# Kernel tuning notes

Measured on AMD Instinct MI355X. Metric: run time of the kernel, lower is better.

Reference implementation:

```python
import jax, jax.numpy as jnp
import numpy as np

B_, L_, H_, N_ = 8, 1024, 1024, 64

def setup_inputs() -> dict:
    key = jax.random.key(0)
    k1, k2, k3, k4 = jax.random.split(key, 4)
    return {
        "samples": jax.random.normal(k1, (B_, L_, 3 * H_), dtype=jnp.float32),
        "label_one_hot": jax.random.uniform(k2, (B_, L_, N_), dtype=jnp.float32),
        "predict": jax.random.normal(k3, (B_, L_, N_), dtype=jnp.float32),
        "W": jax.random.normal(k4, (H_, 3 * H_), dtype=jnp.float32) * (1.0 / np.sqrt(3 * H_)),
        "b_proj": jnp.zeros((H_,), dtype=jnp.float32),
    }

def reference(samples, label_one_hot, predict, W, b_proj):
    # projection: Linear(3H -> H)
    s = jnp.einsum("blk,hk->blh", samples, W) + b_proj          # [b,L,H]
    # dense similarity graph with diagonal masked out, row-softmax
    graph = jnp.einsum("blh,bmh->blm", s, s)                     # [b,L,L]
    L = graph.shape[1]
    eye = jnp.eye(L, dtype=graph.dtype)
    A = jax.nn.softmax(graph - 1e5 * eye, axis=-1)               # [b,L,L]
    # centered masked labels
    sup = label_one_hot
    row_has = (jnp.sum(sup, axis=-1) > 0.5).astype(sup.dtype)    # [b,L]
    total = jnp.sum(row_has, axis=-1)[:, None]                   # [b,1]
    avg = (jnp.sum(sup, axis=-2) / total)[:, None, :]            # [b,1,N]
    B0 = (sup - avg) * row_has[..., None]                        # [b,L,N]
    # diagonal inverse-degree scaling (elementwise, no dense diag matmul)
    d = 1.0 / (jnp.sum(A, axis=-1) + 1e-10)                      # [b,L]
    P = d[:, :, None] * jnp.swapaxes(A, -1, -2)                  # [b,L,L]
    Db = d[:, :, None] * B0                                      # [b,L,N]
    # 6-step power-iteration scan with residual injection at t==3
    ut = jnp.zeros_like(B0)
    for t in range(1, 7):
        ut = jnp.einsum("blm,bmn->bln", P, ut) + Db
        if t == 3:
            ut = ut + predict  # dropout is identity in eval mode
    return ut

if __name__ == "__main__":
    out = reference(**setup_inputs())
    print(out.shape, out.dtype)
```

## Files before the change

kernel.cpp:

```cpp
#include <hip/hip_runtime.h>


typedef _Float16 f16_t;
typedef f16_t f16x4 __attribute__((ext_vector_type(4)));
typedef f16_t f16x8 __attribute__((ext_vector_type(8)));
typedef float floatx4 __attribute__((ext_vector_type(4)));

__device__ __forceinline__ void async_copy16(const void* g, void* l) {
  __builtin_amdgcn_global_load_lds(
      (const __attribute__((address_space(1))) void*)g,
      (__attribute__((address_space(3))) void*)l, 16, 0, 0);
}

__device__ __forceinline__ f16_t hi_of(float x) { return (f16_t)x; }
__device__ __forceinline__ f16_t lo_of(float x, f16_t h) {
  return (f16_t)(x - (float)h);
}

__global__ __launch_bounds__(256) void prep_kernel(
    const float* __restrict__ W, f16_t* __restrict__ Whi, f16_t* __restrict__ Wlo,
    const float* __restrict__ samples, f16_t* __restrict__ SampH)
{
  const int bx = blockIdx.x, tid = threadIdx.x;
  if (bx < 3072) {
    const int i = bx * 256 + tid;
    float4 v = ((const float4*)W)[i];
    v.x *= 32.f; v.y *= 32.f; v.z *= 32.f; v.w *= 32.f;
    f16x4 h, l;
    f16_t h0 = hi_of(v.x); h[0] = h0; l[0] = lo_of(v.x, h0);
    f16_t h1 = hi_of(v.y); h[1] = h1; l[1] = lo_of(v.y, h1);
    f16_t h2 = hi_of(v.z); h[2] = h2; l[2] = lo_of(v.z, h2);
    f16_t h3 = hi_of(v.w); h[3] = h3; l[3] = lo_of(v.w, h3);
    *(f16x4*)(Whi + (size_t)i * 4) = h;
    *(f16x4*)(Wlo + (size_t)i * 4) = l;
  } else {
    const int i = (bx - 3072) * 256 + tid;
    const float4 v = ((const float4*)samples)[i];
    f16x4 h;
    h[0] = (f16_t)v.x; h[1] = (f16_t)v.y; h[2] = (f16_t)v.z; h[3] = (f16_t)v.w;
    *(f16x4*)(SampH + (size_t)i * 4) = h;
  }
}

struct Frags {
  f16x8 a[8];
  f16x8 bh0, bh1, bl0, bl1;
};

#define DSR(dst_, addr_, OFFSTR_) \
  asm volatile("ds_read_b128 %0, %1 offset:" OFFSTR_ : "=v"(dst_) : "v"(addr_))

__device__ __forceinline__ void read_frags_asm(unsigned sa, unsigned sb,
                                               Frags& f) {
  DSR(f.bh0, sb, "0");
  DSR(f.bh1, sb, "1024");
  DSR(f.bl0, sb, "8192");
  DSR(f.bl1, sb, "9216");
  DSR(f.a[0], sa, "0");
  DSR(f.a[1], sa, "1024");
  DSR(f.a[2], sa, "2048");
  DSR(f.a[3], sa, "3072");
  DSR(f.a[4], sa, "4096");
  DSR(f.a[5], sa, "5120");
  DSR(f.a[6], sa, "6144");
  DSR(f.a[7], sa, "7168");
}

__global__ __launch_bounds__(512, 2) void gemm1_pipe(
    const f16_t* __restrict__ Ag,
    const f16_t* __restrict__ BhG, const f16_t* __restrict__ BlG,
    const float* __restrict__ bias,
    f16_t* __restrict__ Chi, f16_t* __restrict__ Clo,
    int N, int K, float cscale)
{
  __shared__ __align__(16) char smem[131072];

  const int tid = threadIdx.x;
  const int lane = tid & 63;
  const int wave = tid >> 6;
  const int wm = wave >> 2;
  const int wn = wave & 3;
  const int bid0 = blockIdx.y * 8 + blockIdx.x;
  const int xk = bid0 & 7, xj = bid0 >> 3;
  const int m0 = ((xk >> 1) * 8 + (xj >> 2)) * 256;
  const int n0 = ((xk & 1) * 4 + (xj & 3)) * 128;
  const int fr = lane & 15;
  const int lch = lane >> 4;

  const int gA0 = tid;
  const int gA1 = tid + 512;
  const int rA0 = gA0 >> 2, lcA0 = (gA0 & 3) ^ ((rA0 >> 1) & 3);
  const int rA1 = gA1 >> 2, lcA1 = (gA1 & 3) ^ ((rA1 >> 1) & 3);
  const int rB = tid >> 2, lcB = (tid & 3) ^ ((rB >> 1) & 3);
  const f16_t* aSrc0 = Ag + (size_t)(m0 + rA0) * K + lcA0 * 8;
  const f16_t* aSrc1 = Ag + (size_t)(m0 + rA1) * K + lcA1 * 8;
  const f16_t* bhSrc = BhG + (size_t)(n0 + rB) * K + lcB * 8;
  const f16_t* blSrc = BlG + (size_t)(n0 + rB) * K + lcB * 8;
  char* ldsA0 = smem + gA0 * 16;
  char* ldsA1 = smem + gA1 * 16;
  char* ldsBh = smem + 16384 + (size_t)tid * 16;
  char* ldsBl = smem + 24576 + (size_t)tid * 16;

  const int swz = (lch ^ ((fr >> 1) & 3)) * 16;
  const int aoff = (wm * 128 + fr) * 64 + swz;
  const int boff = (wn * 32 + fr) * 64 + swz;
  const unsigned ldsBase =
      (unsigned)(size_t)(__attribute__((address_space(3))) char*)smem;
  const unsigned aA0 = ldsBase + (unsigned)aoff;
  const unsigned aA1 = aA0 + 32768u;
  const unsigned aA2 = aA0 + 65536u;
  const unsigned aA3 = aA0 + 98304u;
  const unsigned bA0 = ldsBase + 16384u + (unsigned)boff;
  const unsigned bA1 = bA0 + 32768u;
  const unsigned bA2 = bA0 + 65536u;
  const unsigned bA3 = bA0 + 98304u;

  floatx4 acc[8][2] = {};
  const int NS = K >> 5;

#define STAGE(SS_, SLOT_)                                     \
  do {                                                        \
    int ss = (SS_); if (ss >= NS) ss -= NS;                   \
    const int k0 = ss * 32;                                   \
    async_copy16(aSrc0 + k0, ldsA0 + (SLOT_) * 32768);        \
    async_copy16(aSrc1 + k0, ldsA1 + (SLOT_) * 32768);        \
    async_copy16(bhSrc + k0, ldsBh + (SLOT_) * 32768);        \
    async_copy16(blSrc + k0, ldsBl + (SLOT_) * 32768);        \
  } while (0)

#define MFMA8(F_, P_)                                                                                               \
  do {                                                                                                              \
    acc[2*(P_)][0]   = __builtin_amdgcn_mfma_f32_16x16x32_f16((F_).a[2*(P_)],   (F_).bh0, acc[2*(P_)][0],   0,0,0); \
    acc[2*(P_)][1]   = __builtin_amdgcn_mfma_f32_16x16x32_f16((F_).a[2*(P_)],   (F_).bh1, acc[2*(P_)][1],   0,0,0); \
    acc[2*(P_)+1][0] = __builtin_amdgcn_mfma_f32_16x16x32_f16((F_).a[2*(P_)+1], (F_).bh0, acc[2*(P_)+1][0], 0,0,0); \
    acc[2*(P_)+1][1] = __builtin_amdgcn_mfma_f32_16x16x32_f16((F_).a[2*(P_)+1], (F_).bh1, acc[2*(P_)+1][1], 0,0,0); \
    acc[2*(P_)][0]   = __builtin_amdgcn_mfma_f32_16x16x32_f16((F_).a[2*(P_)],   (F_).bl0, acc[2*(P_)][0],   0,0,0); \
    acc[2*(P_)][1]   = __builtin_amdgcn_mfma_f32_16x16x32_f16((F_).a[2*(P_)],   (F_).bl1, acc[2*(P_)][1],   0,0,0); \
    acc[2*(P_)+1][0] = __builtin_amdgcn_mfma_f32_16x16x32_f16((F_).a[2*(P_)+1], (F_).bl0, acc[2*(P_)+1][0], 0,0,0); \
    acc[2*(P_)+1][1] = __builtin_amdgcn_mfma_f32_16x16x32_f16((F_).a[2*(P_)+1], (F_).bl1, acc[2*(P_)+1][1], 0,0,0); \
  } while (0)

#define SB0 __builtin_amdgcn_sched_barrier(0)

#define HALF(SPRE_, SLOTPRE_, ARD_, BRD_, FRD_, FMM_)            \
  do {                                                           \
    STAGE(SPRE_, SLOTPRE_);                                      \
    asm volatile("s_waitcnt vmcnt(8)" ::: "memory");             \
    __builtin_amdgcn_s_barrier();                                \
    DSR(FRD_.bh0, BRD_, "0");                                    \
    DSR(FRD_.bh1, BRD_, "1024");                                 \
    DSR(FRD_.bl0, BRD_, "8192");                                 \
    SB0;                                                         \
    asm volatile("s_waitcnt lgkmcnt(3)" ::: "memory");           \
    SB0;                                                         \
    __builtin_amdgcn_s_setprio(1);                               \
    MFMA8(FMM_, 0);                                              \
    __builtin_amdgcn_s_setprio(0);                               \
    SB0;                                                         \
    DSR(FRD_.bl1, BRD_, "9216");                                 \
    DSR(FRD_.a[0], ARD_, "0");                                   \
    DSR(FRD_.a[1], ARD_, "1024");                                \
    SB0;                                                         \
    __builtin_amdgcn_s_setprio(1);                               \
    MFMA8(FMM_, 1);                                              \
    __builtin_amdgcn_s_setprio(0);                               \
    SB0;                                                         \
    DSR(FRD_.a[2], ARD_, "2048");                                \
    DSR(FRD_.a[3], ARD_, "3072");                                \
    DSR(FRD_.a[4], ARD_, "4096");                                \
    SB0;                                                         \
    __builtin_amdgcn_s_setprio(1);                               \
    MFMA8(FMM_, 2);                                              \
    __builtin_amdgcn_s_setprio(0);                               \
    SB0;                                                         \
    DSR(FRD_.a[5], ARD_, "5120");                                \
    DSR(FRD_.a[6], ARD_, "6144");                                \
    DSR(FRD_.a[7], ARD_, "7168");                                \
    SB0;                                                         \
    __builtin_amdgcn_s_setprio(1);                               \
    MFMA8(FMM_, 3);                                              \
    __builtin_amdgcn_s_setprio(0);                               \
    SB0;                                                         \
  } while (0)

  Frags f0, f1;

  STAGE(0, 0); STAGE(1, 1); STAGE(2, 2);
  asm volatile("s_waitcnt vmcnt(8)" ::: "memory");
  __builtin_amdgcn_s_barrier();
  read_frags_asm(aA0, bA0, f0);
  SB0;

  for (int s = 0; s < NS; s += 4) {
    HALF(s + 3, 3, aA1, bA1, f1, f0);
    HALF(s + 4, 0, aA2, bA2, f0, f1);
    HALF(s + 5, 1, aA3, bA3, f1, f0);
    HALF(s + 6, 2, aA0, bA0, f0, f1);
  }
  asm volatile("s_waitcnt vmcnt(0)" ::: "memory");
#undef HALF
#undef STAGE
#undef MFMA8

  const int mr = (lane >> 4) * 4;
#pragma unroll
  for (int j = 0; j < 2; ++j) {
    const int n = n0 + wn * 32 + j * 16 + fr;
    const float bj = bias[n];
#pragma unroll
    for (int i = 0; i < 8; ++i) {
#pragma unroll
      for (int r = 0; r < 4; ++r) {
        const int m = m0 + wm * 128 + i * 16 + mr + r;
        float v = acc[i][j][r] * cscale + bj;
        f16_t h = hi_of(v);
        Chi[(size_t)m * N + n] = h;
        Clo[(size_t)m * N + n] = lo_of(v, h);
      }
    }
  }
}

struct Frags2 {
  f16x8 a[4];
  f16x8 bh[4];
  f16x8 bl[4];
};

__global__ __launch_bounds__(256, 2) void gemm2_pipe(
    const f16_t* __restrict__ Sh, const f16_t* __restrict__ Sl,
    float* __restrict__ Gf)
{
  const int K = 1024, N = 1024;
  const long long bo = (long long)blockIdx.z * (1024LL * 1024);
  const f16_t* Ahi = Sh + bo;
  const f16_t* Bhi = Sh + bo;
  const f16_t* Blo = Sl + bo;
  float* Cf = Gf + bo;

  __shared__ __align__(16) char smem[73728];

  const int tid = threadIdx.x;
  const int lane = tid & 63;
  const int wave = tid >> 6;
  const int wm = wave >> 1, wn = wave & 1;

  int idx = blockIdx.x, ti = 0, accu = 0;
  while (accu + ti + 1 <= idx) { accu += ti + 1; ++ti; }
  const int m0 = ti * 128;
  const int n0 = (idx - accu) * 128;

  const int fr = lane & 15;
  const int lch = lane >> 4;

  const int gA0 = tid, gA1 = tid + 256;
  const int rA0 = gA0 >> 2, cA0 = (gA0 & 3) ^ ((rA0 >> 1) & 3);
  const int rA1 = gA1 >> 2, cA1 = (gA1 & 3) ^ ((rA1 >> 1) & 3);
  const f16_t* aSr0 = Ahi + (size_t)(m0 + rA0) * K + cA0 * 8;
  const f16_t* aSr1 = Ahi + (size_t)(m0 + rA1) * K + cA1 * 8;
  const f16_t* hSr0 = Bhi + (size_t)(n0 + rA0) * K + cA0 * 8;
  const f16_t* hSr1 = Bhi + (size_t)(n0 + rA1) * K + cA1 * 8;
  const f16_t* lSr0 = Blo + (size_t)(n0 + rA0) * K + cA0 * 8;
  const f16_t* lSr1 = Blo + (size_t)(n0 + rA1) * K + cA1 * 8;
  char* dA0 = smem + gA0 * 16;
  char* dA1 = smem + gA1 * 16;
  char* dH0 = smem + 8192 + gA0 * 16;
  char* dH1 = smem + 8192 + gA1 * 16;
  char* dL0 = smem + 16384 + gA0 * 16;
  char* dL1 = smem + 16384 + gA1 * 16;

  const int swz16 = (lch ^ ((fr >> 1) & 3)) * 16;
  const int aoff = (wm * 64 + fr) * 64 + swz16;
  const int boff = (wn * 64 + fr) * 64 + swz16;
  const unsigned ldsBase =
      (unsigned)(size_t)(__attribute__((address_space(3))) char*)smem;
  const unsigned aT0 = ldsBase + (unsigned)aoff;
  const unsigned aT1 = aT0 + 24576u;
  const unsigned aT2 = aT0 + 49152u;
  const unsigned bT0 = ldsBase + 8192u + (unsigned)boff;
  const unsigned bT1 = bT0 + 24576u;
  const unsigned bT2 = bT0 + 49152u;

  floatx4 acc[4][4] = {};
  const int NS = 32;

#define STAGE2(SS_, SLOT_)                                    \
  do {                                                        \
    int ss = (SS_); if (ss >= NS) ss -= NS;                   \
    const int k0 = ss * 32;                                   \
    async_copy16(aSr0 + k0, dA0 + (SLOT_) * 24576);           \
    async_copy16(aSr1 + k0, dA1 + (SLOT_) * 24576);           \
    async_copy16(hSr0 + k0, dH0 + (SLOT_) * 24576);           \
    async_copy16(hSr1 + k0, dH1 + (SLOT_) * 24576);           \
    async_copy16(lSr0 + k0, dL0 + (SLOT_) * 24576);           \
    async_copy16(lSr1 + k0, dL1 + (SLOT_) * 24576);           \
  } while (0)

#define MFMA8_2(F_, P_)                                                                              \
  do {                                                                                               \
    acc[0][P_] = __builtin_amdgcn_mfma_f32_16x16x32_f16((F_).a[0], (F_).bh[P_], acc[0][P_], 0,0,0);  \
    acc[1][P_] = __builtin_amdgcn_mfma_f32_16x16x32_f16((F_).a[1], (F_).bh[P_], acc[1][P_], 0,0,0);  \
    acc[2][P_] = __builtin_amdgcn_mfma_f32_16x16x32_f16((F_).a[2], (F_).bh[P_], acc[2][P_], 0,0,0);  \
    acc[3][P_] = __builtin_amdgcn_mfma_f32_16x16x32_f16((F_).a[3], (F_).bh[P_], acc[3][P_], 0,0,0);  \
    acc[0][P_] = __builtin_amdgcn_mfma_f32_16x16x32_f16((F_).a[0], (F_).bl[P_], acc[0][P_], 0,0,0);  \
    acc[1][P_] = __builtin_amdgcn_mfma_f32_16x16x32_f16((F_).a[1], (F_).bl[P_], acc[1][P_], 0,0,0);  \
    acc[2][P_] = __builtin_amdgcn_mfma_f32_16x16x32_f16((F_).a[2], (F_).bl[P_], acc[2][P_], 0,0,0);  \
    acc[3][P_] = __builtin_amdgcn_mfma_f32_16x16x32_f16((F_).a[3], (F_).bl[P_], acc[3][P_], 0,0,0);  \
  } while (0)

#define SB0 __builtin_amdgcn_sched_barrier(0)

#define GR3(SPRE_, SLOTPRE_, ARD_, BRD_, FRD_, FMM_)             \
  do {                                                           \
    STAGE2(SPRE_, SLOTPRE_);                                     \
    asm volatile("s_waitcnt vmcnt(6)" ::: "memory");             \
    __builtin_amdgcn_s_barrier();                                \
    DSR(FRD_.bh[0], BRD_, "0");                                  \
    DSR(FRD_.bh[1], BRD_, "1024");                               \
    DSR(FRD_.bh[2], BRD_, "2048");                               \
    SB0;                                                         \
    asm volatile("s_waitcnt lgkmcnt(3)" ::: "memory");           \
    SB0;                                                         \
    __builtin_amdgcn_s_setprio(1);                               \
    MFMA8_2(FMM_, 0);                                            \
    __builtin_amdgcn_s_setprio(0);                               \
    SB0;                                                         \
    DSR(FRD_.bh[3], BRD_, "3072");                               \
    DSR(FRD_.bl[0], BRD_, "8192");                               \
    DSR(FRD_.bl[1], BRD_, "9216");                               \
    SB0;                                                         \
    __builtin_amdgcn_s_setprio(1);                               \
    MFMA8_2(FMM_, 1);                                            \
    __builtin_amdgcn_s_setprio(0);                               \
    SB0;                                                         \
    DSR(FRD_.bl[2], BRD_, "10240");                              \
    DSR(FRD_.bl[3], BRD_, "11264");                              \
    DSR(FRD_.a[0], ARD_, "0");                                   \
    SB0;                                                         \
    __builtin_amdgcn_s_setprio(1);                               \
    MFMA8_2(FMM_, 2);                                            \
    __builtin_amdgcn_s_setprio(0);                               \
    SB0;                                                         \
    DSR(FRD_.a[1], ARD_, "1024");                                \
    DSR(FRD_.a[2], ARD_, "2048");                                \
    DSR(FRD_.a[3], ARD_, "3072");                                \
    SB0;                                                         \
    __builtin_amdgcn_s_setprio(1);                               \
    MFMA8_2(FMM_, 3);                                            \
    __builtin_amdgcn_s_setprio(0);                               \
    SB0;                                                         \
  } while (0)

  Frags2 f0, f1;

  STAGE2(0, 0); STAGE2(1, 1);
  asm volatile("s_waitcnt vmcnt(6)" ::: "memory");
  __builtin_amdgcn_s_barrier();
  DSR(f0.bh[0], bT0, "0");
  DSR(f0.bh[1], bT0, "1024");
  DSR(f0.bh[2], bT0, "2048");
  DSR(f0.bh[3], bT0, "3072");
  DSR(f0.bl[0], bT0, "8192");
  DSR(f0.bl[1], bT0, "9216");
  DSR(f0.bl[2], bT0, "10240");
  DSR(f0.bl[3], bT0, "11264");
  DSR(f0.a[0], aT0, "0");
  DSR(f0.a[1], aT0, "1024");
  DSR(f0.a[2], aT0, "2048");
  DSR(f0.a[3], aT0, "3072");
  SB0;

  for (int s = 0; s < 30; s += 6) {
    GR3(s + 2, 2, aT1, bT1, f1, f0);
    GR3(s + 3, 0, aT2, bT2, f0, f1);
    GR3(s + 4, 1, aT0, bT0, f1, f0);
    GR3(s + 5, 2, aT1, bT1, f0, f1);
    GR3(s + 6, 0, aT2, bT2, f1, f0);
    GR3(s + 7, 1, aT0, bT0, f0, f1);
  }
  asm volatile("s_waitcnt vmcnt(0)" ::: "memory");
  __builtin_amdgcn_s_barrier();
  DSR(f1.bh[0], bT1, "0");
  DSR(f1.bh[1], bT1, "1024");
  DSR(f1.bh[2], bT1, "2048");
  DSR(f1.bh[3], bT1, "3072");
  DSR(f1.bl[0], bT1, "8192");
  DSR(f1.bl[1], bT1, "9216");
  DSR(f1.bl[2], bT1, "10240");
  DSR(f1.bl[3], bT1, "11264");
  DSR(f1.a[0], aT1, "0");
  DSR(f1.a[1], aT1, "1024");
  DSR(f1.a[2], aT1, "2048");
  DSR(f1.a[3], aT1, "3072");
  SB0;
  asm volatile("s_waitcnt lgkmcnt(12)" ::: "memory");
  SB0;
  __builtin_amdgcn_s_setprio(1);
  MFMA8_2(f0, 0); MFMA8_2(f0, 1); MFMA8_2(f0, 2); MFMA8_2(f0, 3);
  __builtin_amdgcn_s_setprio(0);
  SB0;
  asm volatile("s_waitcnt lgkmcnt(0)" ::: "memory");
  SB0;
  __builtin_amdgcn_s_setprio(1);
  MFMA8_2(f1, 0); MFMA8_2(f1, 1); MFMA8_2(f1, 2); MFMA8_2(f1, 3);
  __builtin_amdgcn_s_setprio(0);
#undef GR3
#undef MFMA8_2
#undef STAGE2

  const int mr = (lane >> 4) * 4;
#pragma unroll
  for (int j = 0; j < 4; ++j) {
    const int n = n0 + wn * 64 + j * 16 + fr;
#pragma unroll
    for (int i = 0; i < 4; ++i) {
#pragma unroll
      for (int r = 0; r < 4; ++r) {
        const int m = m0 + wm * 64 + i * 16 + mr + r;
        float v = acc[i][j][r];
        if (m == n) v -= 1e5f;
        Cf[(size_t)m * N + n] = v;
      }
    }
  }

  if (m0 != n0) {
    float* T = (float*)smem;
#pragma unroll
    for (int mc = 0; mc < 4; ++mc) {
      __syncthreads();
      if (wm == (mc >> 1)) {
        const int ibase = (mc & 1) * 2;
#pragma unroll
        for (int di = 0; di < 2; ++di) {
#pragma unroll
          for (int j = 0; j < 4; ++j) {
            const int nl = wn * 64 + j * 16 + fr;
#pragma unroll
            for (int r = 0; r < 4; ++r) {
              const int mloc = di * 16 + mr + r;
              T[nl * 36 + mloc] = acc[ibase + di][j][r];
            }
          }
        }
      }
      __syncthreads();
      const int row = tid >> 1, half = tid & 1;
      const float* src = &T[row * 36 + half * 16];
      float* dst = Cf + (size_t)(n0 + row) * N + m0 + mc * 32 + half * 16;
#pragma unroll
      for (int q = 0; q < 16; ++q) dst[q] = src[q];
    }
  }
}

__global__ __launch_bounds__(256) void rowstats_kernel(
    const float* __restrict__ G, float* __restrict__ mx, float* __restrict__ inv)
{
  __shared__ float redm[4][4], reds[4][4], mxsh[4];
  const int tid = threadIdx.x;
  const int r0 = blockIdx.x * 4;
  const float* g = G + (size_t)r0 * 1024;
  const float4 v0 = ((const float4*)g)[tid];
  const float4 v1 = ((const float4*)(g + 1024))[tid];
  const float4 v2 = ((const float4*)(g + 2048))[tid];
  const float4 v3 = ((const float4*)(g + 3072))[tid];

  float m0 = fmaxf(fmaxf(v0.x, v0.y), fmaxf(v0.z, v0.w));
  float m1 = fmaxf(fmaxf(v1.x, v1.y), fmaxf(v1.z, v1.w));
  float m2 = fmaxf(fmaxf(v2.x, v2.y), fmaxf(v2.z, v2.w));
  float m3 = fmaxf(fmaxf(v3.x, v3.y), fmaxf(v3.z, v3.w));
#pragma unroll
  for (int off = 32; off > 0; off >>= 1) {
    m0 = fmaxf(m0, __shfl_down(m0, off));
    m1 = fmaxf(m1, __shfl_down(m1, off));
    m2 = fmaxf(m2, __shfl_down(m2, off));
    m3 = fmaxf(m3, __shfl_down(m3, off));
  }
  if ((tid & 63) == 0) {
    redm[0][tid >> 6] = m0; redm[1][tid >> 6] = m1;
    redm[2][tid >> 6] = m2; redm[3][tid >> 6] = m3;
  }
  __syncthreads();
  if (tid < 4)
    mxsh[tid] = fmaxf(fmaxf(redm[tid][0], redm[tid][1]),
                      fmaxf(redm[tid][2], redm[tid][3]));
  __syncthreads();
  const float M0 = mxsh[0], M1 = mxsh[1], M2 = mxsh[2], M3 = mxsh[3];

  float s0 = __expf(v0.x - M0) + __expf(v0.y - M0) + __expf(v0.z - M0) + __expf(v0.w - M0);
  float s1 = __expf(v1.x - M1) + __expf(v1.y - M1) + __expf(v1.z - M1) + __expf(v1.w - M1);
  float s2 = __expf(v2.x - M2) + __expf(v2.y - M2) + __expf(v2.z - M2) + __expf(v2.w - M2);
  float s3 = __expf(v3.x - M3) + __expf(v3.y - M3) + __expf(v3.z - M3) + __expf(v3.w - M3);
#pragma unroll
  for (int off = 32; off > 0; off >>= 1) {
    s0 += __shfl_down(s0, off);
    s1 += __shfl_down(s1, off);
    s2 += __shfl_down(s2, off);
    s3 += __shfl_down(s3, off);
  }
  if ((tid & 63) == 0) {
    reds[0][tid >> 6] = s0; reds[1][tid >> 6] = s1;
    reds[2][tid >> 6] = s2; reds[3][tid >> 6] = s3;
  }
  __syncthreads();
  if (tid < 4) {
    mx[r0 + tid] = mxsh[tid];
    inv[r0 + tid] = 1.0f /
        (reds[tid][0] + reds[tid][1] + reds[tid][2] + reds[tid][3]);
  }
}

__global__ __launch_bounds__(256) void make_at_kernel(
    const float* __restrict__ G, const float* __restrict__ mx,
    const float* __restrict__ inv, f16_t* __restrict__ At)
{
  const int r0 = blockIdx.x * 4;
  const int b = r0 >> 10;
  const int tid = threadIdx.x;
  const float4 m = ((const float4*)(mx + b * 1024))[tid];
  const float4 iv = ((const float4*)(inv + b * 1024))[tid];
#pragma unroll
  for (int k = 0; k < 4; ++k) {
    const float4 g = ((const float4*)(G + (size_t)(r0 + k) * 1024))[tid];
    f16x4 o;
    o[0] = (f16_t)(__expf(g.x - m.x) * iv.x);
    o[1] = (f16_t)(__expf(g.y - m.y) * iv.y);
    o[2] = (f16_t)(__expf(g.z - m.z) * iv.z);
    o[3] = (f16_t)(__expf(g.w - m.w) * iv.w);
    *(f16x4*)(At + (size_t)(r0 + k) * 1024 + tid * 4) = o;
  }
}

__global__ __launch_bounds__(256) void db_stats(
    const float* __restrict__ sup, float* __restrict__ colpart,
    float* __restrict__ totalpart)
{
  const int b = blockIdx.x >> 4, chunk = blockIdx.x & 15;
  const int tid = threadIdx.x;
  const int r = tid >> 2, q = tid & 3;
  const float* s = sup + ((size_t)b * 1024 + chunk * 64 + r) * 64 + q * 16;
  const float4 x0 = ((const float4*)s)[0];
  const float4 x1 = ((const float4*)s)[1];
  const float4 x2 = ((const float4*)s)[2];
  const float4 x3 = ((const float4*)s)[3];

  float rs = (x0.x + x0.y + x0.z + x0.w) + (x1.x + x1.y + x1.z + x1.w) +
             (x2.x + x2.y + x2.z + x2.w) + (x3.x + x3.y + x3.z + x3.w);
  rs += __shfl_xor(rs, 1);
  rs += __shfl_xor(rs, 2);
  const float rh = (rs > 0.5f) ? 1.f : 0.f;

  __shared__ float colp[64];
  __shared__ float tp[4];
  if (tid < 64) colp[tid] = 0.f;
  __syncthreads();
  atomicAdd(&colp[q * 16 + 0], x0.x);  atomicAdd(&colp[q * 16 + 1], x0.y);
  atomicAdd(&colp[q * 16 + 2], x0.z);  atomicAdd(&colp[q * 16 + 3], x0.w);
  atomicAdd(&colp[q * 16 + 4], x1.x);  atomicAdd(&colp[q * 16 + 5], x1.y);
  atomicAdd(&colp[q * 16 + 6], x1.z);  atomicAdd(&colp[q * 16 + 7], x1.w);
  atomicAdd(&colp[q * 16 + 8], x2.x);  atomicAdd(&colp[q * 16 + 9], x2.y);
  atomicAdd(&colp[q * 16 + 10], x2.z); atomicAdd(&colp[q * 16 + 11], x2.w);
  atomicAdd(&colp[q * 16 + 12], x3.x); atomicAdd(&colp[q * 16 + 13], x3.y);
  atomicAdd(&colp[q * 16 + 14], x3.z); atomicAdd(&colp[q * 16 + 15], x3.w);

  float ts = (q == 0) ? rh : 0.f;
#pragma unroll
  for (int off = 32; off > 0; off >>= 1) ts += __shfl_down(ts, off);
  if ((tid & 63) == 0) tp[tid >> 6] = ts;
  __syncthreads();
  if (tid < 64) colpart[((size_t)b * 16 + chunk) * 64 + tid] = colp[tid];
  if (tid == 0) totalpart[b * 16 + chunk] = tp[0] + tp[1] + tp[2] + tp[3];
}

__global__ __launch_bounds__(256) void db_apply(
    const float* __restrict__ sup, const float* __restrict__ colpart,
    const float* __restrict__ totalpart,
    float* __restrict__ Db, f16_t* __restrict__ DbT)
{
  const int b = blockIdx.x >> 4, chunk = blockIdx.x & 15;
  const int tid = threadIdx.x;
  const int r = tid >> 2, q = tid & 3;

  __shared__ float avgsh[64];
  __shared__ float totsh;
  __shared__ f16_t DbTs[64 * 72];

  float a = 0.f;
  if (tid < 64) {
#pragma unroll
    for (int c = 0; c < 16; ++c) a += colpart[((size_t)b * 16 + c) * 64 + tid];
  }
  if (tid == 0) {
    float tt = 0.f;
#pragma unroll
    for (int c = 0; c < 16; ++c) tt += totalpart[b * 16 + c];
    totsh = tt;
  }
  __syncthreads();
  if (tid < 64) avgsh[tid] = a / totsh;
  __syncthreads();

  const size_t rowoff = ((size_t)b * 1024 + chunk * 64 + r) * 64 + q * 16;
  const float* s = sup + rowoff;
  float4 x0 = ((const float4*)s)[0];
  float4 x1 = ((const float4*)s)[1];
  float4 x2 = ((const float4*)s)[2];
  float4 x3 = ((const float4*)s)[3];

  float rs = (x0.x + x0.y + x0.z + x0.w) + (x1.x + x1.y + x1.z + x1.w) +
             (x2.x + x2.y + x2.z + x2.w) + (x3.x + x3.y + x3.z + x3.w);
  rs += __shfl_xor(rs, 1);
  rs += __shfl_xor(rs, 2);
  const float rh = (rs > 0.5f) ? 1.f : 0.f;

  const int nb = q * 16;
  x0.x = (x0.x - avgsh[nb + 0]) * rh;  x0.y = (x0.y - avgsh[nb + 1]) * rh;
  x0.z = (x0.z - avgsh[nb + 2]) * rh;  x0.w = (x0.w - avgsh[nb + 3]) * rh;
  x1.x = (x1.x - avgsh[nb + 4]) * rh;  x1.y = (x1.y - avgsh[nb + 5]) * rh;
  x1.z = (x1.z - avgsh[nb + 6]) * rh;  x1.w = (x1.w - avgsh[nb + 7]) * rh;
  x2.x = (x2.x - avgsh[nb + 8]) * rh;  x2.y = (x2.y - avgsh[nb + 9]) * rh;
  x2.z = (x2.z - avgsh[nb + 10]) * rh; x2.w = (x2.w - avgsh[nb + 11]) * rh;
  x3.x = (x3.x - avgsh[nb + 12]) * rh; x3.y = (x3.y - avgsh[nb + 13]) * rh;
  x3.z = (x3.z - avgsh[nb + 14]) * rh; x3.w = (x3.w - avgsh[nb + 15]) * rh;

  float* d = Db + rowoff;
  ((float4*)d)[0] = x0; ((float4*)d)[1] = x1;
  ((float4*)d)[2] = x2; ((float4*)d)[3] = x3;

  DbTs[(nb + 0) * 72 + r] = (f16_t)x0.x;  DbTs[(nb + 1) * 72 + r] = (f16_t)x0.y;
  DbTs[(nb + 2) * 72 + r] = (f16_t)x0.z;  DbTs[(nb + 3) * 72 + r] = (f16_t)x0.w;
  DbTs[(nb + 4) * 72 + r] = (f16_t)x1.x;  DbTs[(nb + 5) * 72 + r] = (f16_t)x1.y;
  DbTs[(nb + 6) * 72 + r] = (f16_t)x1.z;  DbTs[(nb + 7) * 72 + r] = (f16_t)x1.w;
  DbTs[(nb + 8) * 72 + r] = (f16_t)x2.x;  DbTs[(nb + 9) * 72 + r] = (f16_t)x2.y;
  DbTs[(nb + 10) * 72 + r] = (f16_t)x2.z; DbTs[(nb + 11) * 72 + r] = (f16_t)x2.w;
  DbTs[(nb + 12) * 72 + r] = (f16_t)x3.x; DbTs[(nb + 13) * 72 + r] = (f16_t)x3.y;
  DbTs[(nb + 14) * 72 + r] = (f16_t)x3.z; DbTs[(nb + 15) * 72 + r] = (f16_t)x3.w;
  __syncthreads();

  const int n = tid >> 2, seg = tid & 3;
  const f16_t* src = &DbTs[n * 72 + seg * 16];
  f16_t* dst = DbT + ((size_t)b * 64 + n) * 1024 + chunk * 64 + seg * 16;
  *(f16x8*)dst = *(const f16x8*)src;
  *(f16x8*)(dst + 8) = *(const f16x8*)(src + 8);
}

template <int PRED, int FINAL>
__global__ __launch_bounds__(256) void iter_step(
    const f16_t* __restrict__ At, const f16_t* __restrict__ UT,
    const float* __restrict__ Db, const float* __restrict__ Pred,
    f16_t* __restrict__ UTn, float* __restrict__ OutF)
{
  const int L = 1024, Nn = 64;
  const int b = blockIdx.y, l0 = blockIdx.x * 32;
  At += (size_t)b * L * L;
  UT += (size_t)b * Nn * L;

  __shared__ __align__(16) char smem[131072];

  const int tid = threadIdx.x;
  const int lane = tid & 63;
  const int wave = tid >> 6;
  const int fr = lane & 15;
  const int lch = lane >> 4;
  const int mwb = wave * 256;

  int g_, rw_, sc_;
  g_ = lane;        rw_ = g_ >> 3; sc_ = (g_ & 7) ^ (rw_ & 7);
  const f16_t* aS0 = At + (size_t)(l0 + rw_) * L + mwb + sc_ * 8;
  g_ = lane + 64;   rw_ = g_ >> 3; sc_ = (g_ & 7) ^ (rw_ & 7);
  const f16_t* aS1 = At + (size_t)(l0 + rw_) * L + mwb + sc_ * 8;
  g_ = lane + 128;  rw_ = g_ >> 3; sc_ = (g_ & 7) ^ (rw_ & 7);
  const f16_t* aS2 = At + (size_t)(l0 + rw_) * L + mwb + sc_ * 8;
  g_ = lane + 192;  rw_ = g_ >> 3; sc_ = (g_ & 7) ^ (rw_ & 7);
  const f16_t* aS3 = At + (size_t)(l0 + rw_) * L + mwb + sc_ * 8;
  g_ = lane;        rw_ = g_ >> 3; sc_ = (g_ & 7) ^ (rw_ & 7);
  const f16_t* uS0 = UT + (size_t)rw_ * L + mwb + sc_ * 8;
  g_ = lane + 64;   rw_ = g_ >> 3; sc_ = (g_ & 7) ^ (rw_ & 7);
  const f16_t* uS1 = UT + (size_t)rw_ * L + mwb + sc_ * 8;
  g_ = lane + 128;  rw_ = g_ >> 3; sc_ = (g_ & 7) ^ (rw_ & 7);
  const f16_t* uS2 = UT + (size_t)rw_ * L + mwb + sc_ * 8;
  g_ = lane + 192;  rw_ = g_ >> 3; sc_ = (g_ & 7) ^ (rw_ & 7);
  const f16_t* uS3 = UT + (size_t)rw_ * L + mwb + sc_ * 8;
  g_ = lane + 256;  rw_ = g_ >> 3; sc_ = (g_ & 7) ^ (rw_ & 7);
  const f16_t* uS4 = UT + (size_t)rw_ * L + mwb + sc_ * 8;
  g_ = lane + 320;  rw_ = g_ >> 3; sc_ = (g_ & 7) ^ (rw_ & 7);
  const f16_t* uS5 = UT + (size_t)rw_ * L + mwb + sc_ * 8;
  g_ = lane + 384;  rw_ = g_ >> 3; sc_ = (g_ & 7) ^ (rw_ & 7);
  const f16_t* uS6 = UT + (size_t)rw_ * L + mwb + sc_ * 8;
  g_ = lane + 448;  rw_ = g_ >> 3; sc_ = (g_ & 7) ^ (rw_ & 7);
  const f16_t* uS7 = UT + (size_t)rw_ * L + mwb + sc_ * 8;

  char* stA = smem + wave * 24576;
  char* stU = stA + 4096;

  const int offK0 = fr * 128 + ((lch ^ (fr & 7)) * 16);
  const int offK1 = fr * 128 + (((4 + lch) ^ (fr & 7)) * 16);

  floatx4 acc[2][4] = {};

#define STG(M0_, BUF_)                                        \
  do {                                                        \
    char* dA = stA + (BUF_) * 12288;                          \
    char* dU = stU + (BUF_) * 12288;                          \
    async_copy16(aS0 + (M0_), dA + lane * 16);                \
    async_copy16(aS1 + (M0_), dA + 1024 + lane * 16);         \
    async_copy16(aS2 + (M0_), dA + 2048 + lane * 16);         \
    async_copy16(aS3 + (M0_), dA + 3072 + lane * 16);         \
    async_copy16(uS0 + (M0_), dU + lane * 16);                \
    async_copy16(uS1 + (M0_), dU + 1024 + lane * 16);         \
    async_copy16(uS2 + (M0_), dU + 2048 + lane * 16);         \
    async_copy16(uS3 + (M0_), dU + 3072 + lane * 16);         \
    async_copy16(uS4 + (M0_), dU + 4096 + lane * 16);         \
    async_copy16(uS5 + (M0_), dU + 5120 + lane * 16);         \
    async_copy16(uS6 + (M0_), dU + 6144 + lane * 16);         \
    async_copy16(uS7 + (M0_), dU + 7168 + lane * 16);         \
  } while (0)

#define LD8(b_, o_) (*(const f16x8*)((b_) + (o_)))
#define MM(A_, U_, C_) C_ = __builtin_amdgcn_mfma_f32_16x16x32_f16(A_, U_, C_, 0, 0, 0)

#define CHUNK(BUF_)                                                       \
  do {                                                                    \
    const char* cA = stA + (BUF_) * 12288;                                \
    const char* cU = stU + (BUF_) * 12288;                                \
    f16x8 a00 = LD8(cA, offK0), a01 = LD8(cA, offK1);                     \
    f16x8 a10 = LD8(cA, offK0 + 2048), a11 = LD8(cA, offK1 + 2048);       \
    f16x8 u00 = LD8(cU, offK0), u01 = LD8(cU, offK1);                     \
    f16x8 u10 = LD8(cU, offK0 + 2048), u11 = LD8(cU, offK1 + 2048);       \
    f16x8 u20 = LD8(cU, offK0 + 4096), u21 = LD8(cU, offK1 + 4096);       \
    f16x8 u30 = LD8(cU, offK0 + 6144), u31 = LD8(cU, offK1 + 6144);       \
    MM(a00, u00, acc[0][0]); MM(a00, u10, acc[0][1]);                     \
    MM(a00, u20, acc[0][2]); MM(a00, u30, acc[0][3]);                     \
    MM(a10, u00, acc[1][0]); MM(a10, u10, acc[1][1]);                     \
    MM(a10, u20, acc[1][2]); MM(a10, u30, acc[1][3]);                     \
    MM(a01, u01, acc[0][0]); MM(a01, u11, acc[0][1]);                     \
    MM(a01, u21, acc[0][2]); MM(a01, u31, acc[0][3]);                     \
    MM(a11, u01, acc[1][0]); MM(a11, u11, acc[1][1]);                     \
    MM(a11, u21, acc[1][2]); MM(a11, u31, acc[1][3]);                     \
  } while (0)

#define SB0 __builtin_amdgcn_sched_barrier(0)

  STG(0, 0);
  STG(64, 1);
  asm volatile("s_waitcnt vmcnt(12)" ::: "memory");
  SB0;
  CHUNK(0);
  SB0;
  STG(128, 0);
  asm volatile("s_waitcnt vmcnt(12)" ::: "memory");
  SB0;
  CHUNK(1);
  SB0;
  STG(192, 1);
  asm volatile("s_waitcnt vmcnt(12)" ::: "memory");
  SB0;
  CHUNK(0);
  SB0;
  asm volatile("s_waitcnt vmcnt(0)" ::: "memory");
  SB0;
  CHUNK(1);
#undef CHUNK
#undef STG

  float* P = (float*)(smem + 98304) + wave * 2048;
  const int mr = (lane >> 4) * 4;
#pragma unroll
  for (int li = 0; li < 2; ++li)
#pragma unroll
    for (int j = 0; j < 4; ++j)
#pragma unroll
      for (int r = 0; r < 4; ++r)
        P[(li * 16 + mr + r) * 64 + j * 16 + fr] = acc[li][j][r];
  __syncthreads();

  const float* P0 = (const float*)(smem + 98304);
  const size_t obase = ((size_t)b * L + l0) * Nn;
  f16_t* OutS = (f16_t*)smem;
#pragma unroll
  for (int it = 0; it < 2; ++it) {
    const int e4 = it * 256 + tid;
    const int l = e4 >> 4, n4 = (e4 & 15) * 4;
    const int eo = l * 64 + n4;
    float4 v = *(const float4*)(P0 + eo);
    const float4 p1 = *(const float4*)(P0 + 2048 + eo);
    const float4 p2 = *(const float4*)(P0 + 4096 + eo);
    const float4 p3 = *(const float4*)(P0 + 6144 + eo);
    v.x += p1.x; v.y += p1.y; v.z += p1.z; v.w += p1.w;
    v.x += p2.x; v.y += p2.y; v.z += p2.z; v.w += p2.w;
    v.x += p3.x; v.y += p3.y; v.z += p3.z; v.w += p3.w;
    const float4 d = *(const float4*)(Db + obase + eo);
    v.x += d.x; v.y += d.y; v.z += d.z; v.w += d.w;
    if (PRED) {
      const float4 p = *(const float4*)(Pred + obase + eo);
      v.x += p.x; v.y += p.y; v.z += p.z; v.w += p.w;
    }
    if (FINAL) {
      *(float4*)(OutF + obase + eo) = v;
    } else {
      OutS[(n4 + 0) * 40 + l] = (f16_t)v.x;
      OutS[(n4 + 1) * 40 + l] = (f16_t)v.y;
      OutS[(n4 + 2) * 40 + l] = (f16_t)v.z;
      OutS[(n4 + 3) * 40 + l] = (f16_t)v.w;
    }
  }
  if (!FINAL) {
    __syncthreads();
    f16_t* dst = UTn + (size_t)b * Nn * L + l0;
    const int n = tid >> 2, lc = (tid & 3) * 8;
    *(f16x8*)(dst + (size_t)n * L + lc) = *(const f16x8*)&OutS[n * 40 + lc];
  }
#undef SB0
#undef LD8
#undef MM
}

extern "C" void kernel_launch(void* const* d_in, const int* in_sizes, int n_in,
                              void* d_out, int out_size, void* d_ws, size_t ws_size,
                              hipStream_t stream) {
  const float* samples = (const float*)d_in[0];
  const float* label   = (const float*)d_in[1];
  const float* predict = (const float*)d_in[2];
  const float* W       = (const float*)d_in[3];
  const float* bproj   = (const float*)d_in[4];
  float* out = (float*)d_out;

  char* ws = (char*)d_ws;
  f16_t* Whi = (f16_t*)ws;
  f16_t* Wlo = (f16_t*)(ws + 6291456);
  float* mx  = (float*)ws;
  float* inv = (float*)(ws + 32768);
  float* Db  = (float*)(ws + 65536);
  f16_t* DbT = (f16_t*)(ws + 65536 + 2097152);
  f16_t* UTa = (f16_t*)(ws + 65536 + 3145728);
  f16_t* UTb = (f16_t*)(ws + 65536 + 4194304);
  float* colpart   = (float*)(ws + 5308416);
  float* totalpart = (float*)(ws + 5308416 + 32768);
  f16_t* SampH = (f16_t*)(ws + 12582912);
  float* G     = (float*)(ws + 12582912);
  f16_t* Shi = (f16_t*)(ws + 62914560);
  f16_t* Slo = (f16_t*)(ws + 62914560 + 16777216);
  f16_t* At  = Shi;

  prep_kernel<<<dim3(27648), 256, 0, stream>>>(W, Whi, Wlo, samples, SampH);

  gemm1_pipe<<<dim3(8, 32), 512, 0, stream>>>(
      SampH, Whi, Wlo, bproj, Shi, Slo, 1024, 3072, 1.0f / 32.0f);

  gemm2_pipe<<<dim3(36, 1, 8), 256, 0, stream>>>(Shi, Slo, G);

  rowstats_kernel<<<2048, 256, 0, stream>>>(G, mx, inv);
  make_at_kernel<<<2048, 256, 0, stream>>>(G, mx, inv, At);

  db_stats<<<128, 256, 0, stream>>>(label, colpart, totalpart);
  db_apply<<<128, 256, 0, stream>>>(label, colpart, totalpart, Db, DbT);

  dim3 gi(32, 8);
  iter_step<0, 0><<<gi, 256, 0, stream>>>(At, DbT, Db, nullptr, UTa, nullptr);
  iter_step<1, 0><<<gi, 256, 0, stream>>>(At, UTa, Db, predict, UTb, nullptr);
  iter_step<0, 0><<<gi, 256, 0, stream>>>(At, UTb, Db, nullptr, UTa, nullptr);
  iter_step<0, 0><<<gi, 256, 0, stream>>>(At, UTa, Db, nullptr, UTb, nullptr);
  iter_step<0, 1><<<gi, 256, 0, stream>>>(At, UTb, Db, nullptr, nullptr, out);
}
```

Baseline: 353.8 us.

## Retile projection GEMM to 128x128 tiles with 3-stage pipeline and 4 waves

The projection GEMM moves from 256x128 tiles with 8 waves and a 4-slot LDS ring to 128x128 tiles with 4 waves and a 3-slot ring, raising the grid from 256 to 512 blocks so more of the CUs get work. Each wave now computes a 64x64 sub-tile as a 4x4 accumulator grid, and the block-to-tile mapping is rewritten with an XCD-aware swizzle. The trade-off is lower arithmetic intensity per block, since A is reused across fewer B columns, and a shallower prefetch depth.

```diff
diff --git a/kernel.cpp b/kernel.cpp
--- a/kernel.cpp
+++ b/kernel.cpp
@@ -42,176 +42,177 @@
   }
 }
 
-struct Frags {
-  f16x8 a[8];
-  f16x8 bh0, bh1, bl0, bl1;
-};
-
 #define DSR(dst_, addr_, OFFSTR_) \
   asm volatile("ds_read_b128 %0, %1 offset:" OFFSTR_ : "=v"(dst_) : "v"(addr_))
 
-__device__ __forceinline__ void read_frags_asm(unsigned sa, unsigned sb,
-                                               Frags& f) {
-  DSR(f.bh0, sb, "0");
-  DSR(f.bh1, sb, "1024");
-  DSR(f.bl0, sb, "8192");
-  DSR(f.bl1, sb, "9216");
-  DSR(f.a[0], sa, "0");
-  DSR(f.a[1], sa, "1024");
-  DSR(f.a[2], sa, "2048");
-  DSR(f.a[3], sa, "3072");
-  DSR(f.a[4], sa, "4096");
-  DSR(f.a[5], sa, "5120");
-  DSR(f.a[6], sa, "6144");
-  DSR(f.a[7], sa, "7168");
-}
-
-__global__ __launch_bounds__(512, 2) void gemm1_pipe(
+struct Frags2 {
+  f16x8 a[4];
+  f16x8 bh[4];
+  f16x8 bl[4];
+};
+
+__global__ __launch_bounds__(256, 2) void gemm1_pipe(
     const f16_t* __restrict__ Ag,
     const f16_t* __restrict__ BhG, const f16_t* __restrict__ BlG,
     const float* __restrict__ bias,
     f16_t* __restrict__ Chi, f16_t* __restrict__ Clo,
     int N, int K, float cscale)
 {
-  __shared__ __align__(16) char smem[131072];
+  __shared__ __align__(16) char smem[73728];
 
   const int tid = threadIdx.x;
   const int lane = tid & 63;
   const int wave = tid >> 6;
-  const int wm = wave >> 2;
-  const int wn = wave & 3;
-  const int bid0 = blockIdx.y * 8 + blockIdx.x;
-  const int xk = bid0 & 7, xj = bid0 >> 3;
-  const int m0 = ((xk >> 1) * 8 + (xj >> 2)) * 256;
-  const int n0 = ((xk & 1) * 4 + (xj & 3)) * 128;
+  const int wm = wave >> 1, wn = wave & 1;
+
+  const int bid = blockIdx.x;
+  const int xcd = bid & 7, idx = bid >> 3;
+  const int m0 = (xcd * 8 + (idx >> 3)) * 128;
+  const int n0 = (idx & 7) * 128;
+
   const int fr = lane & 15;
   const int lch = lane >> 4;
 
-  const int gA0 = tid;
-  const int gA1 = tid + 512;
-  const int rA0 = gA0 >> 2, lcA0 = (gA0 & 3) ^ ((rA0 >> 1) & 3);
-  const int rA1 = gA1 >> 2, lcA1 = (gA1 & 3) ^ ((rA1 >> 1) & 3);
-  const int rB = tid >> 2, lcB = (tid & 3) ^ ((rB >> 1) & 3);
-  const f16_t* aSrc0 = Ag + (size_t)(m0 + rA0) * K + lcA0 * 8;
-  const f16_t* aSrc1 = Ag + (size_t)(m0 + rA1) * K + lcA1 * 8;
-  const f16_t* bhSrc = BhG + (size_t)(n0 + rB) * K + lcB * 8;
-  const f16_t* blSrc = BlG + (size_t)(n0 + rB) * K + lcB * 8;
-  char* ldsA0 = smem + gA0 * 16;
-  char* ldsA1 = smem + gA1 * 16;
-  char* ldsBh = smem + 16384 + (size_t)tid * 16;
-  char* ldsBl = smem + 24576 + (size_t)tid * 16;
-
-  const int swz = (lch ^ ((fr >> 1) & 3)) * 16;
-  const int aoff = (wm * 128 + fr) * 64 + swz;
-  const int boff = (wn * 32 + fr) * 64 + swz;
+  const int gA0 = tid, gA1 = tid + 256;
+  const int rA0 = gA0 >> 2, cA0 = (gA0 & 3) ^ ((rA0 >> 1) & 3);
+  const int rA1 = gA1 >> 2, cA1 = (gA1 & 3) ^ ((rA1 >> 1) & 3);
+  const f16_t* aSr0 = Ag + (size_t)(m0 + rA0) * K + cA0 * 8;
+  const f16_t* aSr1 = Ag + (size_t)(m0 + rA1) * K + cA1 * 8;
+  const f16_t* hSr0 = BhG + (size_t)(n0 + rA0) * K + cA0 * 8;
+  const f16_t* hSr1 = BhG + (size_t)(n0 + rA1) * K + cA1 * 8;
+  const f16_t* lSr0 = BlG + (size_t)(n0 + rA0) * K + cA0 * 8;
+  const f16_t* lSr1 = BlG + (size_t)(n0 + rA1) * K + cA1 * 8;
+  char* dA0 = smem + gA0 * 16;
+  char* dA1 = smem + gA1 * 16;
+  char* dH0 = smem + 8192 + gA0 * 16;
+  char* dH1 = smem + 8192 + gA1 * 16;
+  char* dL0 = smem + 16384 + gA0 * 16;
+  char* dL1 = smem + 16384 + gA1 * 16;
+
+  const int swz16 = (lch ^ ((fr >> 1) & 3)) * 16;
+  const int aoff = (wm * 64 + fr) * 64 + swz16;
+  const int boff = (wn * 64 + fr) * 64 + swz16;
   const unsigned ldsBase =
       (unsigned)(size_t)(__attribute__((address_space(3))) char*)smem;
-  const unsigned aA0 = ldsBase + (unsigned)aoff;
-  const unsigned aA1 = aA0 + 32768u;
-  const unsigned aA2 = aA0 + 65536u;
-  const unsigned aA3 = aA0 + 98304u;
-  const unsigned bA0 = ldsBase + 16384u + (unsigned)boff;
-  const unsigned bA1 = bA0 + 32768u;
-  const unsigned bA2 = bA0 + 65536u;
-  const unsigned bA3 = bA0 + 98304u;
-
-  floatx4 acc[8][2] = {};
+  const unsigned aT0 = ldsBase + (unsigned)aoff;
+  const unsigned aT1 = aT0 + 24576u;
+  const unsigned aT2 = aT0 + 49152u;
+  const unsigned bT0 = ldsBase + 8192u + (unsigned)boff;
+  const unsigned bT1 = bT0 + 24576u;
+  const unsigned bT2 = bT0 + 49152u;
+
+  floatx4 acc[4][4] = {};
   const int NS = K >> 5;
 
-#define STAGE(SS_, SLOT_)                                     \
+#define STAGE1(SS_, SLOT_)                                    \
   do {                                                        \
     int ss = (SS_); if (ss >= NS) ss -= NS;                   \
     const int k0 = ss * 32;                                   \
-    async_copy16(aSrc0 + k0, ldsA0 + (SLOT_) * 32768);        \
-    async_copy16(aSrc1 + k0, ldsA1 + (SLOT_) * 32768);        \
-    async_copy16(bhSrc + k0, ldsBh + (SLOT_) * 32768);        \
-    async_copy16(blSrc + k0, ldsBl + (SLOT_) * 32768);        \
+    async_copy16(aSr0 + k0, dA0 + (SLOT_) * 24576);           \
+    async_copy16(aSr1 + k0, dA1 + (SLOT_) * 24576);           \
+    async_copy16(hSr0 + k0, dH0 + (SLOT_) * 24576);           \
+    async_copy16(hSr1 + k0, dH1 + (SLOT_) * 24576);           \
+    async_copy16(lSr0 + k0, dL0 + (SLOT_) * 24576);           \
+    async_copy16(lSr1 + k0, dL1 + (SLOT_) * 24576);           \
   } while (0)
 
-#define MFMA8(F_, P_)                                                                                               \
-  do {                                                                                                              \
-    acc[2*(P_)][0]   = __builtin_amdgcn_mfma_f32_16x16x32_f16((F_).a[2*(P_)],   (F_).bh0, acc[2*(P_)][0],   0,0,0); \
-    acc[2*(P_)][1]   = __builtin_amdgcn_mfma_f32_16x16x32_f16((F_).a[2*(P_)],   (F_).bh1, acc[2*(P_)][1],   0,0,0); \
-    acc[2*(P_)+1][0] = __builtin_amdgcn_mfma_f32_16x16x32_f16((F_).a[2*(P_)+1], (F_).bh0, acc[2*(P_)+1][0], 0,0,0); \
-    acc[2*(P_)+1][1] = __builtin_amdgcn_mfma_f32_16x16x32_f16((F_).a[2*(P_)+1], (F_).bh1, acc[2*(P_)+1][1], 0,0,0); \
-    acc[2*(P_)][0]   = __builtin_amdgcn_mfma_f32_16x16x32_f16((F_).a[2*(P_)],   (F_).bl0, acc[2*(P_)][0],   0,0,0); \
-    acc[2*(P_)][1]   = __builtin_amdgcn_mfma_f32_16x16x32_f16((F_).a[2*(P_)],   (F_).bl1, acc[2*(P_)][1],   0,0,0); \
-    acc[2*(P_)+1][0] = __builtin_amdgcn_mfma_f32_16x16x32_f16((F_).a[2*(P_)+1], (F_).bl0, acc[2*(P_)+1][0], 0,0,0); \
-    acc[2*(P_)+1][1] = __builtin_amdgcn_mfma_f32_16x16x32_f16((F_).a[2*(P_)+1], (F_).bl1, acc[2*(P_)+1][1], 0,0,0); \
+#define MFMA8_1(F_, P_)                                                                              \
+  do {                                                                                               \
+    acc[0][P_] = __builtin_amdgcn_mfma_f32_16x16x32_f16((F_).a[0], (F_).bh[P_], acc[0][P_], 0,0,0);  \
+    acc[1][P_] = __builtin_amdgcn_mfma_f32_16x16x32_f16((F_).a[1], (F_).bh[P_], acc[1][P_], 0,0,0);  \
+    acc[2][P_] = __builtin_amdgcn_mfma_f32_16x16x32_f16((F_).a[2], (F_).bh[P_], acc[2][P_], 0,0,0);  \
+    acc[3][P_] = __builtin_amdgcn_mfma_f32_16x16x32_f16((F_).a[3], (F_).bh[P_], acc[3][P_], 0,0,0);  \
+    acc[0][P_] = __builtin_amdgcn_mfma_f32_16x16x32_f16((F_).a[0], (F_).bl[P_], acc[0][P_], 0,0,0);  \
+    acc[1][P_] = __builtin_amdgcn_mfma_f32_16x16x32_f16((F_).a[1], (F_).bl[P_], acc[1][P_], 0,0,0);  \
+    acc[2][P_] = __builtin_amdgcn_mfma_f32_16x16x32_f16((F_).a[2], (F_).bl[P_], acc[2][P_], 0,0,0);  \
+    acc[3][P_] = __builtin_amdgcn_mfma_f32_16x16x32_f16((F_).a[3], (F_).bl[P_], acc[3][P_], 0,0,0);  \
   } while (0)
 
 #define SB0 __builtin_amdgcn_sched_barrier(0)
 
-#define HALF(SPRE_, SLOTPRE_, ARD_, BRD_, FRD_, FMM_)            \
+#define GR1(SPRE_, SLOTPRE_, ARD_, BRD_, FRD_, FMM_)             \
   do {                                                           \
-    STAGE(SPRE_, SLOTPRE_);                                      \
-    asm volatile("s_waitcnt vmcnt(8)" ::: "memory");             \
+    STAGE1(SPRE_, SLOTPRE_);                                     \
+    asm volatile("s_waitcnt vmcnt(6)" ::: "memory");             \
     __builtin_amdgcn_s_barrier();                                \
-    DSR(FRD_.bh0, BRD_, "0");                                    \
-    DSR(FRD_.bh1, BRD_, "1024");                                 \
-    DSR(FRD_.bl0, BRD_, "8192");                                 \
+    DSR(FRD_.bh[0], BRD_, "0");                                  \
+    DSR(FRD_.bh[1], BRD_, "1024");                               \
+    DSR(FRD_.bh[2], BRD_, "2048");                               \
     SB0;                                                         \
     asm volatile("s_waitcnt lgkmcnt(3)" ::: "memory");           \
     SB0;                                                         \
     __builtin_amdgcn_s_setprio(1);                               \
-    MFMA8(FMM_, 0);                                              \
+    MFMA8_1(FMM_, 0);                                            \
     __builtin_amdgcn_s_setprio(0);                               \
     SB0;                                                         \
-    DSR(FRD_.bl1, BRD_, "9216");                                 \
+    DSR(FRD_.bh[3], BRD_, "3072");                               \
+    DSR(FRD_.bl[0], BRD_, "8192");                               \
+    DSR(FRD_.bl[1], BRD_, "9216");                               \
+    SB0;                                                         \
+    __builtin_amdgcn_s_setprio(1);                               \
+    MFMA8_1(FMM_, 1);                                            \
+    __builtin_amdgcn_s_setprio(0);                               \
+    SB0;                                                         \
+    DSR(FRD_.bl[2], BRD_, "10240");                              \
+    DSR(FRD_.bl[3], BRD_, "11264");                              \
     DSR(FRD_.a[0], ARD_, "0");                                   \
+    SB0;                                                         \
+    __builtin_amdgcn_s_setprio(1);                               \
+    MFMA8_1(FMM_, 2);                                            \
+    __builtin_amdgcn_s_setprio(0);                               \
+    SB0;                                                         \
     DSR(FRD_.a[1], ARD_, "1024");                                \
-    SB0;                                                         \
-    __builtin_amdgcn_s_setprio(1);                               \
-    MFMA8(FMM_, 1);                                              \
-    __builtin_amdgcn_s_setprio(0);                               \
-    SB0;                                                         \
     DSR(FRD_.a[2], ARD_, "2048");                                \
     DSR(FRD_.a[3], ARD_, "3072");                                \
-    DSR(FRD_.a[4], ARD_, "4096");                                \
     SB0;                                                         \
     __builtin_amdgcn_s_setprio(1);                               \
-    MFMA8(FMM_, 2);                                              \
+    MFMA8_1(FMM_, 3);                                            \
     __builtin_amdgcn_s_setprio(0);                               \
     SB0;                                                         \
-    DSR(FRD_.a[5], ARD_, "5120");                                \
-    DSR(FRD_.a[6], ARD_, "6144");                                \
-    DSR(FRD_.a[7], ARD_, "7168");                                \
-    SB0;                                                         \
-    __builtin_amdgcn_s_setprio(1);                               \
-    MFMA8(FMM_, 3);                                              \
-    __builtin_amdgcn_s_setprio(0);                               \
-    SB0;                                                         \
   } while (0)
 
-  Frags f0, f1;
-
-  STAGE(0, 0); STAGE(1, 1); STAGE(2, 2);
-  asm volatile("s_waitcnt vmcnt(8)" ::: "memory");
+  Frags2 f0, f1;
+
+  STAGE1(0, 0); STAGE1(1, 1);
+  asm volatile("s_waitcnt vmcnt(6)" ::: "memory");
   __builtin_amdgcn_s_barrier();
-  read_frags_asm(aA0, bA0, f0);
-  SB0;
-
-  for (int s = 0; s < NS; s += 4) {
-    HALF(s + 3, 3, aA1, bA1, f1, f0);
-    HALF(s + 4, 0, aA2, bA2, f0, f1);
-    HALF(s + 5, 1, aA3, bA3, f1, f0);
-    HALF(s + 6, 2, aA0, bA0, f0, f1);
+  DSR(f0.bh[0], bT0, "0");
+  DSR(f0.bh[1], bT0, "1024");
+  DSR(f0.bh[2], bT0, "2048");
+  DSR(f0.bh[3], bT0, "3072");
+  DSR(f0.bl[0], bT0, "8192");
+  DSR(f0.bl[1], bT0, "9216");
+  DSR(f0.bl[2], bT0, "10240");
+  DSR(f0.bl[3], bT0, "11264");
+  DSR(f0.a[0], aT0, "0");
+  DSR(f0.a[1], aT0, "1024");
+  DSR(f0.a[2], aT0, "2048");
+  DSR(f0.a[3], aT0, "3072");
+  SB0;
+
+  for (int s = 0; s < NS; s += 6) {
+    GR1(s + 2, 2, aT1, bT1, f1, f0);
+    GR1(s + 3, 0, aT2, bT2, f0, f1);
+    GR1(s + 4, 1, aT0, bT0, f1, f0);
+    GR1(s + 5, 2, aT1, bT1, f0, f1);
+    GR1(s + 6, 0, aT2, bT2, f1, f0);
+    GR1(s + 7, 1, aT0, bT0, f0, f1);
   }
   asm volatile("s_waitcnt vmcnt(0)" ::: "memory");
-#undef HALF
-#undef STAGE
-#undef MFMA8
+#undef GR1
+#undef MFMA8_1
+#undef STAGE1
 
   const int mr = (lane >> 4) * 4;
 #pragma unroll
-  for (int j = 0; j < 2; ++j) {
-    const int n = n0 + wn * 32 + j * 16 + fr;
+  for (int j = 0; j < 4; ++j) {
+    const int n = n0 + wn * 64 + j * 16 + fr;
     const float bj = bias[n];
 #pragma unroll
-    for (int i = 0; i < 8; ++i) {
+    for (int i = 0; i < 4; ++i) {
 #pragma unroll
       for (int r = 0; r < 4; ++r) {
-        const int m = m0 + wm * 128 + i * 16 + mr + r;
+        const int m = m0 + wm * 64 + i * 16 + mr + r;
         float v = acc[i][j][r] * cscale + bj;
         f16_t h = hi_of(v);
         Chi[(size_t)m * N + n] = h;
@@ -220,12 +221,6 @@
     }
   }
 }
-
-struct Frags2 {
-  f16x8 a[4];
-  f16x8 bh[4];
-  f16x8 bl[4];
-};
 
 __global__ __launch_bounds__(256, 2) void gemm2_pipe(
     const f16_t* __restrict__ Sh, const f16_t* __restrict__ Sl,
@@ -845,7 +840,7 @@
 
   prep_kernel<<<dim3(27648), 256, 0, stream>>>(W, Whi, Wlo, samples, SampH);
 
-  gemm1_pipe<<<dim3(8, 32), 512, 0, stream>>>(
+  gemm1_pipe<<<dim3(512), 256, 0, stream>>>(
       SampH, Whi, Wlo, bproj, Shi, Slo, 1024, 3072, 1.0f / 32.0f);
 
   gemm2_pipe<<<dim3(36, 1, 8), 256, 0, stream>>>(Shi, Slo, G);
```

New measurement: 372.7 us. 1.05x slower.
